# Kernel optimization log

Measured on AMD Instinct MI355X. Metric: run time of the kernel, lower is better.

Reference implementation:

```python
import jax, jax.numpy as jnp
import numpy as np

HEADS = 8
DIM_HEAD = 64
CHUNK = 128
EPS = 1e-6
KERNEL_EPS = 1e-4


def softmax_kernel(x, proj, is_query):
    # x: [b,h,n,d], proj: [f,d]  (FAVOR+ positive softmax features)
    d = x.shape[-1]
    data_normalizer = d ** -0.25
    ratio = proj.shape[0] ** -0.5
    data_dash = jnp.einsum('bhnd,fd->bhnf', x * data_normalizer, proj)
    diag = 0.5 * (data_normalizer ** 2) * jnp.sum(x * x, axis=-1, keepdims=True)  # [b,h,n,1]
    if is_query:
        m = jnp.max(data_dash, axis=-1, keepdims=True)
    else:
        m = jnp.max(data_dash, axis=(-1, -2), keepdims=True)
    return ratio * (jnp.exp(data_dash - diag - jax.lax.stop_gradient(m)) + KERNEL_EPS)


def infer_hidden_states(q, k, v, chunk_size=CHUNK):
    # q,k: [b,h,n,f], v: [b,h,n,e]; chunked causal linear attention with carried cumsums
    b, h, n, f = q.shape
    e = v.shape[-1]
    nc = n // chunk_size

    def to_chunks(t):
        return jnp.moveaxis(t.reshape(b, h, nc, chunk_size, t.shape[-1]), 2, 0)

    qs, ks, vs = to_chunks(q), to_chunks(k), to_chunks(v)

    def step(carry, inp):
        Z, S = carry  # [b,h,1,f], [b,h,1,f,e]
        qc, kc, vc = inp
        k_cum = Z + jnp.cumsum(kc, axis=2)                       # [b,h,c,f]
        D_inv = 1.0 / jnp.einsum('bhnf,bhnf->bhn', qc, k_cum + EPS)
        ctx = jnp.einsum('bhnf,bhne->bhnfe', kc, vc)             # [b,h,c,f,e]
        ctx_cum = S + jnp.cumsum(ctx, axis=2)
        out = jnp.einsum('bhnfe,bhnf,bhn->bhne', ctx_cum, qc, D_inv)
        return (k_cum[:, :, -1:], ctx_cum[:, :, -1:]), out

    init = (jnp.zeros((b, h, 1, f), q.dtype), jnp.zeros((b, h, 1, f, e), q.dtype))
    (Z, S), outs = jax.lax.scan(step, init, (qs, ks, vs))
    out = jnp.moveaxis(outs, 0, 2).reshape(b, h, n, e)
    return out, Z[:, :, 0], S[:, :, 0]


def reference(x, proj, Wq, Wk, Wv, Wo, bo):
    b, n, dim = x.shape
    h, dh = HEADS, DIM_HEAD

    def split_heads(t):
        return jnp.transpose(t.reshape(b, n, h, dh), (0, 2, 1, 3))

    q = split_heads(x @ Wq)
    k = split_heads(x @ Wk)
    v = split_heads(x @ Wv)

    qf = softmax_kernel(q, proj, is_query=True)
    kf = softmax_kernel(k, proj, is_query=False)

    out, Z, S = infer_hidden_states(qf, kf, v)
    out = jnp.transpose(out, (0, 2, 1, 3)).reshape(b, n, h * dh)
    out = out @ Wo + bo
    return out, Z, S


def setup_inputs() -> dict:
    key = jax.random.key(0)
    ks = jax.random.split(key, 6)
    b, n, dim = 2, 2048, 512
    f = 256
    return {
        'x': jax.random.normal(ks[0], (b, n, dim), jnp.float32),
        'proj': jax.random.normal(ks[1], (f, DIM_HEAD), jnp.float32),
        'Wq': jax.random.normal(ks[2], (dim, dim), jnp.float32) * (dim ** -0.5),
        'Wk': jax.random.normal(ks[3], (dim, dim), jnp.float32) * (dim ** -0.5),
        'Wv': jax.random.normal(ks[4], (dim, dim), jnp.float32) * (dim ** -0.5),
        'Wo': jax.random.normal(ks[5], (dim, dim), jnp.float32) * (dim ** -0.5),
        'bo': jnp.zeros((dim,), jnp.float32),
    }
```

## Files before the change

### kernel.cpp

```cpp
#include <hip/hip_runtime.h>
#include <hip/hip_bf16.h>
#include <math.h>

#define NB    2
#define NSEQ  2048
#define DIMM  512
#define NH    8
#define DHd   64
#define FF    256
#define CHK   128
#define NCHK  16
#define NBH   16

typedef unsigned short ushort_t;
typedef __attribute__((ext_vector_type(8))) __bf16 bf16x8;
typedef __attribute__((ext_vector_type(4))) float floatx4;

__device__ __forceinline__ unsigned short f2bf(float x) {
    union { __hip_bfloat16 h; unsigned short u; } v;
    v.h = __float2bfloat16(x);
    return v.u;
}
__device__ __forceinline__ float bf2f(unsigned short u) {
    union { unsigned short u2[2]; float f; } v;
    v.u2[0] = 0; v.u2[1] = u;
    return v.f;
}
__device__ __forceinline__ unsigned enc_f(float x) {
    unsigned u = __float_as_uint(x);
    return (u & 0x80000000u) ? ~u : (u | 0x80000000u);
}
__device__ __forceinline__ float dec_f(unsigned e) {
    unsigned u = (e & 0x80000000u) ? (e & 0x7fffffffu) : ~e;
    return __uint_as_float(u);
}

__device__ __forceinline__ void gload16(const void* g, void* l) {
    __builtin_amdgcn_global_load_lds(
        (const __attribute__((address_space(1))) void*)g,
        (__attribute__((address_space(3))) void*)l, 16, 0, 0);
}

__device__ __forceinline__ bf16x8 frag8(const ushort_t* lds, int row, int kb) {
    return *((const bf16x8*)lds + row * 8 + (kb ^ (row & 7)));
}
__device__ __forceinline__ bf16x8 fragS(const ushort_t* lds, int row, int kb) {
    return *((const bf16x8*)lds + row * 16 + (kb ^ (row & 15)));
}

__device__ __forceinline__ void stage8(const ushort_t* __restrict__ G, ushort_t* dst,
                                       int ld, int tid) {
#pragma unroll
    for (int t = 0; t < 4; t++) {
        const int g = t * 256 + tid, r = g >> 3, kb = (g & 7) ^ (r & 7);
        gload16(G + (size_t)r * ld + kb * 8, dst + (size_t)g * 8);
    }
}
__device__ __forceinline__ void stage4h(const ushort_t* __restrict__ G, ushort_t* dst,
                                        int ld, int tid) {
#pragma unroll
    for (int t = 0; t < 2; t++) {
        const int g = t * 256 + tid, r = g >> 3, kb = (g & 7) ^ (r & 7);
        gload16(G + (size_t)r * ld + kb * 8, dst + (size_t)g * 8);
    }
}
__device__ __forceinline__ void stageV(const ushort_t* __restrict__ G, ushort_t* dst,
                                       int tid) {
#pragma unroll
    for (int t = 0; t < 4; t++) {
        const int g = t * 256 + tid, r = g >> 4, kb = (g & 15) ^ (r & 15);
        gload16(G + (size_t)r * NSEQ + kb * 8, dst + (size_t)g * 8);
    }
}

__global__ __launch_bounds__(256)
void prep(const float* __restrict__ x, const float* __restrict__ proj,
          const float* __restrict__ W0, const float* __restrict__ W1,
          const float* __restrict__ W2, const float* __restrict__ W3,
          ushort_t* __restrict__ xb, ushort_t* __restrict__ projb,
          ushort_t* __restrict__ T0, ushort_t* __restrict__ T1,
          ushort_t* __restrict__ T2, ushort_t* __restrict__ T3,
          unsigned* __restrict__ mk_u)
{
    __shared__ float t[32][33];
    const int b = blockIdx.x, tid = threadIdx.x;
    if (b < 2048) {
        const int gid = b * 256 + tid;
        const float4 v = *(const float4*)(x + (size_t)gid * 4);
        union { ushort4 v4; unsigned short s[4]; } pk;
        pk.s[0] = f2bf(v.x); pk.s[1] = f2bf(v.y); pk.s[2] = f2bf(v.z); pk.s[3] = f2bf(v.w);
        ((ushort4*)xb)[gid] = pk.v4;
    } else if (b < 2064) {
        const int gid = (b - 2048) * 256 + tid;
        const float dn = 0.35355339059327379f;
        const float4 v = *(const float4*)(proj + (size_t)gid * 4);
        union { ushort4 v4; unsigned short s[4]; } pk;
        pk.s[0] = f2bf(v.x * dn); pk.s[1] = f2bf(v.y * dn);
        pk.s[2] = f2bf(v.z * dn); pk.s[3] = f2bf(v.w * dn);
        ((ushort4*)projb)[gid] = pk.v4;
    } else if (b < 3088) {
        const int idx = b - 2064;
        const int z = idx >> 8, rem = idx & 255;
        const int bx = rem & 15, by = rem >> 4;
        const float* W = (z == 0) ? W0 : (z == 1) ? W1 : (z == 2) ? W2 : W3;
        ushort_t* T = (z == 0) ? T0 : (z == 1) ? T1 : (z == 2) ? T2 : T3;
        const int x0 = bx * 32, y0 = by * 32;
        const int tx = tid & 31, ty = tid >> 5;
#pragma unroll
        for (int i = 0; i < 4; i++)
            t[ty + i * 8][tx] = W[(size_t)(y0 + ty + i * 8) * DIMM + x0 + tx];
        __syncthreads();
#pragma unroll
        for (int i = 0; i < 4; i++)
            T[(size_t)(x0 + ty + i * 8) * DIMM + y0 + tx] = f2bf(t[tx][ty + i * 8]);
    } else {
        if (tid < NBH) mk_u[tid] = 0u;
    }
}

__device__ __forceinline__ void mm44(const ushort_t* A, const ushort_t* B,
                                     floatx4 acc[4][4], int wm, int wn, int c, int q)
{
#pragma unroll
    for (int ks = 0; ks < 2; ks++) {
        bf16x8 af[4], bfr[4];
#pragma unroll
        for (int i = 0; i < 4; i++) {
            af[i]  = frag8(A, wm + i * 16 + c, ks * 4 + q);
            bfr[i] = frag8(B, wn + i * 16 + c, ks * 4 + q);
        }
#pragma unroll
        for (int i = 0; i < 4; i++)
#pragma unroll
            for (int j = 0; j < 4; j++)
                acc[i][j] = __builtin_amdgcn_mfma_f32_16x16x32_bf16(
                    af[i], bfr[j], acc[i][j], 0, 0, 0);
    }
}

__global__ __launch_bounds__(256)
void gemm_qkv(const ushort_t* __restrict__ xb,
              const ushort_t* __restrict__ Wtq, const ushort_t* __restrict__ Wtk,
              const ushort_t* __restrict__ Wtv, const ushort_t* __restrict__ projb,
              ushort_t* __restrict__ qb, ushort_t* __restrict__ kb,
              ushort_t* __restrict__ vTb, unsigned* __restrict__ mk_u)
{
    __shared__ alignas(16) ushort_t SM[33792];
    __shared__ float wred[2][4];
    ushort_t* A0 = SM;
    ushort_t* B0 = SM + 8192;
    ushort_t* A1 = SM + 16384;
    ushort_t* B1 = SM + 24576;
    ushort_t* PS = SM + 17408;
    const int tid = threadIdx.x;
    const int bid = blockIdx.x;
    const int z = bid % 3, tt = bid / 3;
    const int n0 = (tt & 3) * 128, m0 = (tt >> 2) * 128;
    const ushort_t* Bt = (z == 0) ? Wtq : ((z == 1) ? Wtk : Wtv);
    const ushort_t* AG = xb + (size_t)m0 * DIMM;
    const ushort_t* BG = Bt + (size_t)n0 * DIMM;

    const int lane = tid & 63, wid = tid >> 6;
    const int q = lane >> 4, cl = lane & 15;
    const int wm = (wid >> 1) * 64, wn = (wid & 1) * 64;

    floatx4 zero = {0.f, 0.f, 0.f, 0.f};
    floatx4 acc[4][4];
#pragma unroll
    for (int i = 0; i < 4; i++)
#pragma unroll
        for (int j = 0; j < 4; j++) acc[i][j] = zero;

    stage8(AG, A0, DIMM, tid);
    stage8(BG, B0, DIMM, tid);
    __syncthreads();
    for (int t4 = 0; t4 < 4; t4++) {
        const int k0 = t4 * 128;
        stage8(AG + k0 + 64, A1, DIMM, tid);
        stage8(BG + k0 + 64, B1, DIMM, tid);
        mm44(A0, B0, acc, wm, wn, cl, q);
        __syncthreads();
        if (t4 < 3) {
            stage8(AG + k0 + 128, A0, DIMM, tid);
            stage8(BG + k0 + 128, B0, DIMM, tid);
        }
        mm44(A1, B1, acc, wm, wn, cl, q);
        __syncthreads();
    }

    if (z == 1) {
        stage8(projb, PS, 64, tid);
        stage8(projb + 8192, PS + 8192, 64, tid);
    }

#pragma unroll
    for (int i = 0; i < 4; i++)
#pragma unroll
        for (int j = 0; j < 4; j++) {
            const int col = wn + j * 16 + cl;
#pragma unroll
            for (int r = 0; r < 4; r++) {
                const int row = wm + i * 16 + q * 4 + r;
                SM[row * 136 + col] = f2bf(acc[i][j][r]);
            }
        }
    __syncthreads();

    if (z < 2) {
        ushort_t* ob = (z == 0) ? qb : kb;
#pragma unroll
        for (int p = 0; p < 16; p++) {
            const int idx = p * 256 + tid;
            const int row = idx >> 5, c4 = idx & 31;
            ushort4 o = *(const ushort4*)&SM[row * 136 + c4 * 4];
            *(ushort4*)(ob + (size_t)(m0 + row) * DIMM + n0 + c4 * 4) = o;
        }
        if (z == 1) {
            const int bb = m0 >> 11;
            const int h0 = n0 >> 6;
            float mx[2] = {-3.0e38f, -3.0e38f};
#pragma unroll
            for (int hh = 0; hh < 2; hh++) {
#pragma unroll
                for (int half = 0; half < 2; half++) {
                    floatx4 a2[4][4];
#pragma unroll
                    for (int i = 0; i < 4; i++)
#pragma unroll
                        for (int j = 0; j < 4; j++) a2[i][j] = zero;
#pragma unroll
                    for (int ks = 0; ks < 2; ks++) {
                        bf16x8 af[4], bfr[4];
#pragma unroll
                        for (int i = 0; i < 4; i++)
                            af[i] = *(const bf16x8*)&SM[(wm + i * 16 + cl) * 136 + hh * 64 + (ks * 4 + q) * 8];
#pragma unroll
                        for (int j = 0; j < 4; j++)
                            bfr[j] = frag8(PS + half * 8192, wn + j * 16 + cl, ks * 4 + q);
#pragma unroll
                        for (int i = 0; i < 4; i++)
#pragma unroll
                            for (int j = 0; j < 4; j++)
                                a2[i][j] = __builtin_amdgcn_mfma_f32_16x16x32_bf16(
                                    af[i], bfr[j], a2[i][j], 0, 0, 0);
                    }
#pragma unroll
                    for (int i = 0; i < 4; i++)
#pragma unroll
                        for (int j = 0; j < 4; j++)
#pragma unroll
                            for (int r = 0; r < 4; r++) mx[hh] = fmaxf(mx[hh], a2[i][j][r]);
                }
            }
#pragma unroll
            for (int hh = 0; hh < 2; hh++) {
                float m = mx[hh];
                m = fmaxf(m, __shfl_xor(m, 1));  m = fmaxf(m, __shfl_xor(m, 2));
                m = fmaxf(m, __shfl_xor(m, 4));  m = fmaxf(m, __shfl_xor(m, 8));
                m = fmaxf(m, __shfl_xor(m, 16)); m = fmaxf(m, __shfl_xor(m, 32));
                if (lane == 0) wred[hh][wid] = m;
            }
            __syncthreads();
            if (tid == 0) {
#pragma unroll
                for (int hh = 0; hh < 2; hh++) {
                    const float m = fmaxf(fmaxf(wred[hh][0], wred[hh][1]),
                                          fmaxf(wred[hh][2], wred[hh][3]));
                    atomicMax(&mk_u[bb * NH + h0 + hh], enc_f(m));
                }
            }
        }
    } else {
        const int bb = m0 >> 11, nbase = m0 & 2047;
#pragma unroll
        for (int p = 0; p < 16; p++) {
            const int idx = p * 256 + tid;
            const int cl2 = idx >> 5, n4 = idx & 31;
            const int C = n0 + cl2;
            const int h = C >> 6, e = C & 63;
            union { ushort4 v4; unsigned short s[4]; } pk;
#pragma unroll
            for (int k = 0; k < 4; k++) pk.s[k] = SM[(n4 * 4 + k) * 136 + cl2];
            *(ushort4*)(vTb + (((size_t)(bb * NH + h) * 64 + e)) * NSEQ + nbase + n4 * 4) = pk.v4;
        }
    }
}

__device__ __forceinline__ void mm24(const ushort_t* A, const ushort_t* B,
                                     floatx4 acc[2][4], int wm, int wn, int c, int q)
{
#pragma unroll
    for (int ks = 0; ks < 2; ks++) {
        bf16x8 af[2], bfr[4];
#pragma unroll
        for (int i = 0; i < 2; i++) af[i] = frag8(A, wm + i * 16 + c, ks * 4 + q);
#pragma unroll
        for (int j = 0; j < 4; j++) bfr[j] = frag8(B, wn + j * 16 + c, ks * 4 + q);
#pragma unroll
        for (int i = 0; i < 2; i++)
#pragma unroll
            for (int j = 0; j < 4; j++)
                acc[i][j] = __builtin_amdgcn_mfma_f32_16x16x32_bf16(
                    af[i], bfr[j], acc[i][j], 0, 0, 0);
    }
}

__global__ __launch_bounds__(256)
void gemm_out(const ushort_t* __restrict__ attnb, const ushort_t* __restrict__ Wto,
              float* __restrict__ out, const float* __restrict__ bias)
{
    __shared__ alignas(16) ushort_t A0[4096];
    __shared__ alignas(16) ushort_t A1[4096];
    __shared__ alignas(16) ushort_t B0[8192];
    __shared__ alignas(16) ushort_t B1[8192];
    const int tid = threadIdx.x;
    const int n0 = blockIdx.x * 128, m0 = blockIdx.y * 64;
    const ushort_t* AG = attnb + (size_t)m0 * DIMM;
    const ushort_t* BG = Wto + (size_t)n0 * DIMM;

    floatx4 zero = {0.f, 0.f, 0.f, 0.f};
    floatx4 acc[2][4];
#pragma unroll
    for (int i = 0; i < 2; i++)
#pragma unroll
        for (int j = 0; j < 4; j++) acc[i][j] = zero;

    const int lane = tid & 63, wid = tid >> 6;
    const int q = lane >> 4, c = lane & 15;
    const int wm = (wid >> 1) * 32, wn = (wid & 1) * 64;

    stage4h(AG, A0, DIMM, tid);
    stage8(BG, B0, DIMM, tid);
    __syncthreads();
    for (int tt = 0; tt < 4; tt++) {
        const int k0 = tt * 128;
        stage4h(AG + k0 + 64, A1, DIMM, tid);
        stage8(BG + k0 + 64, B1, DIMM, tid);
        mm24(A0, B0, acc, wm, wn, c, q);
        __syncthreads();
        if (tt < 3) {
            stage4h(AG + k0 + 128, A0, DIMM, tid);
            stage8(BG + k0 + 128, B0, DIMM, tid);
        }
        mm24(A1, B1, acc, wm, wn, c, q);
        __syncthreads();
    }

#pragma unroll
    for (int i = 0; i < 2; i++)
#pragma unroll
        for (int j = 0; j < 4; j++) {
            const int col = n0 + wn + j * 16 + c;
            const float bv = bias[col];
#pragma unroll
            for (int r = 0; r < 4; r++) {
                const int row = m0 + wm + i * 16 + q * 4 + r;
                out[(size_t)row * DIMM + col] = acc[i][j][r] + bv;
            }
        }
}

__global__ __launch_bounds__(256)
void featk(const ushort_t* __restrict__ kb_, const ushort_t* __restrict__ projb,
           const unsigned* __restrict__ mk_u, const ushort_t* __restrict__ vTb,
           ushort_t* __restrict__ kfb, float* __restrict__ CTXT,
           float* __restrict__ Ksum)
{
    __shared__ alignas(16) ushort_t SM[17408];
    __shared__ alignas(16) ushort_t Vs[8192];
    __shared__ float dtmp[256];
    __shared__ float diag_l[128];
    __shared__ float colp[2][128];
    ushort_t* As = SM;
    ushort_t* Bs = SM + 8192;
    const int tid = threadIdx.x, lane = tid & 63, wid = tid >> 6;
    const int q = lane >> 4, cl = lane & 15;
    const int m0 = blockIdx.x * 128, h = blockIdx.y, fh = blockIdx.z;
    const int bb = m0 >> 11, nloc = m0 & 2047;
    const int bh = bb * NH + h;
    const int cidx = nloc >> 7;
    const ushort_t* Aq = kb_ + (size_t)m0 * DIMM + h * 64;
    const ushort_t* Vg = vTb + ((size_t)bh * 64) * NSEQ + nloc;
    const ushort_t* Pj = projb + (size_t)fh * 128 * 64;

    {
        const int row = tid >> 1, half = tid & 1;
        float s = 0.f;
        const ushort_t* p = Aq + (size_t)row * DIMM + half * 32;
#pragma unroll
        for (int d = 0; d < 32; d += 4) {
            ushort4 w = *(const ushort4*)(p + d);
            float a = bf2f(w.x), b2 = bf2f(w.y), c2 = bf2f(w.z), d2 = bf2f(w.w);
            s += a * a + b2 * b2 + c2 * c2 + d2 * d2;
        }
        dtmp[tid] = s;
    }
    stage8(Aq, As, DIMM, tid);
    stage8(Pj, Bs, 64, tid);
    stageV(Vg, Vs, tid);
    __syncthreads();
    if (tid < 128) diag_l[tid] = (dtmp[2 * tid] + dtmp[2 * tid + 1]) * 0.0625f;

    floatx4 zero = {0.f, 0.f, 0.f, 0.f};
    floatx4 acc[4][4];
#pragma unroll
    for (int i = 0; i < 4; i++)
#pragma unroll
        for (int j = 0; j < 4; j++) acc[i][j] = zero;
    const int wm = (wid >> 1) * 64, wn = (wid & 1) * 64;
#pragma unroll
    for (int ks = 0; ks < 2; ks++) {
        bf16x8 af[4], bfr[4];
#pragma unroll
        for (int i = 0; i < 4; i++) af[i] = frag8(As, wm + i * 16 + cl, ks * 4 + q);
#pragma unroll
        for (int j = 0; j < 4; j++) bfr[j] = frag8(Bs, wn + j * 16 + cl, ks * 4 + q);
#pragma unroll
        for (int i = 0; i < 4; i++)
#pragma unroll
            for (int j = 0; j < 4; j++)
                acc[i][j] = __builtin_amdgcn_mfma_f32_16x16x32_bf16(
                    af[i], bfr[j], acc[i][j], 0, 0, 0);
    }
    __syncthreads();

    const float mk = dec_f(mk_u[bh]);
#pragma unroll
    for (int i = 0; i < 4; i++)
#pragma unroll
        for (int r = 0; r < 4; r++) {
            const int row = wm + i * 16 + q * 4 + r;
            const float cc = diag_l[row] + mk;
#pragma unroll
            for (int j = 0; j < 4; j++)
                acc[i][j][r] = 0.0625f * (__expf(acc[i][j][r] - cc) + 1.0e-4f);
        }

#pragma unroll
    for (int j = 0; j < 4; j++) {
        float s = 0.f;
#pragma unroll
        for (int i = 0; i < 4; i++)
            s += acc[i][j][0] + acc[i][j][1] + acc[i][j][2] + acc[i][j][3];
        s += __shfl_xor(s, 16);
        s += __shfl_xor(s, 32);
        if (q == 0) colp[wid >> 1][wn + j * 16 + cl] = s;
    }

#pragma unroll
    for (int i = 0; i < 4; i++)
#pragma unroll
        for (int j = 0; j < 4; j++) {
            const int col = wn + j * 16 + cl;
#pragma unroll
            for (int r = 0; r < 4; r++) {
                const int row = wm + i * 16 + q * 4 + r;
                SM[row * 136 + col] = f2bf(acc[i][j][r]);
            }
        }
    __syncthreads();

    if (tid < 128)
        Ksum[((size_t)bh * NCHK + cidx) * FF + fh * 128 + tid] = colp[0][tid] + colp[1][tid];

    const size_t frow = (size_t)bh * NSEQ + nloc;
#pragma unroll
    for (int p = 0; p < 16; p++) {
        const int idx = p * 256 + tid;
        const int row = idx >> 5, c4 = idx & 31;
        ushort4 o = *(const ushort4*)&SM[row * 136 + c4 * 4];
        *(ushort4*)(kfb + (frow + row) * FF + fh * 128 + c4 * 4) = o;
    }
    __syncthreads();

    ushort_t* T = SM;
    const size_t cbase = ((size_t)bh * NCHK + cidx) * 64;
#pragma unroll
    for (int fq = 0; fq < 2; fq++) {
        if ((wid & 1) == fq) {
#pragma unroll
            for (int jj = 0; jj < 4; jj++) {
#pragma unroll
                for (int i = 0; i < 4; i++)
#pragma unroll
                    for (int r = 0; r < 4; r++) {
                        const int n = wm + i * 16 + q * 4 + r;
                        T[(jj * 16 + cl) * 136 + n] = f2bf(acc[i][jj][r]);
                    }
            }
        }
        __syncthreads();
        floatx4 accc[4];
#pragma unroll
        for (int jj = 0; jj < 4; jj++) accc[jj] = zero;
#pragma unroll
        for (int kt = 0; kt < 4; kt++) {
            const bf16x8 av = fragS(Vs, wid * 16 + cl, kt * 4 + q);
#pragma unroll
            for (int jj = 0; jj < 4; jj++) {
                const bf16x8 bv = *(const bf16x8*)(T + (jj * 16 + cl) * 136 + (kt * 4 + q) * 8);
                accc[jj] = __builtin_amdgcn_mfma_f32_16x16x32_bf16(av, bv, accc[jj], 0, 0, 0);
            }
        }
#pragma unroll
        for (int jj = 0; jj < 4; jj++) {
            const int f = fh * 128 + fq * 64 + jj * 16 + cl;
#pragma unroll
            for (int r = 0; r < 4; r++) {
                const int e = wid * 16 + q * 4 + r;
                CTXT[(cbase + e) * FF + f] = accc[jj][r];
            }
        }
        __syncthreads();
    }
}

__global__ void prefix_zs(float* __restrict__ Ksum, float* __restrict__ Zout,
                          const float* __restrict__ CTXT, ushort_t* __restrict__ ctxp,
                          float* __restrict__ Sout)
{
    const int b = blockIdx.x;
    if (b < 1024) {
        const int idx = b * 256 + threadIdx.x;
        const int bh = idx >> 14, ef = idx & 16383;
        const int e = ef >> 8, f = ef & 255;
        float run = 0.f;
#pragma unroll
        for (int c = 0; c < NCHK; c++) {
            const size_t o = (((size_t)bh * NCHK + c) * 64 + e) * FF + f;
            const float t = CTXT[o];
            ctxp[o] = f2bf(run);
            run += t;
        }
        Sout[((size_t)bh * FF + f) * 64 + e] = run;
    } else {
        const int idx = (b - 1024) * 256 + threadIdx.x;
        const int bh = idx >> 8, f = idx & 255;
        float run = 0.f;
#pragma unroll
        for (int c = 0; c < NCHK; c++) {
            const size_t o = ((size_t)(bh * NCHK + c)) * FF + f;
            const float t = Ksum[o];
            Ksum[o] = run;
            run += t;
        }
        Zout[(size_t)bh * FF + f] = run;
    }
}

template<int NJ>
__device__ __forceinline__ void st1N(const ushort_t* QFs, const ushort_t* Bk,
                                     floatx4* acc1, int wv, int cl, int q)
{
#pragma unroll
    for (int ks = 0; ks < 2; ks++) {
        const bf16x8 af = frag8(QFs, wv * 16 + cl, ks * 4 + q);
        bf16x8 bfr[NJ];
#pragma unroll
        for (int j = 0; j < NJ; j++) bfr[j] = frag8(Bk, j * 16 + cl, ks * 4 + q);
#pragma unroll
        for (int j = 0; j < NJ; j++)
            acc1[j] = __builtin_amdgcn_mfma_f32_16x16x32_bf16(af, bfr[j], acc1[j], 0, 0, 0);
    }
}

__device__ __forceinline__ void pv4(const ushort_t* CpB, const ushort_t* QFs,
                                    floatx4 acc2[4], int wv, int cl, int q)
{
#pragma unroll
    for (int ks = 0; ks < 2; ks++) {
        const bf16x8 bfr = frag8(QFs, wv * 16 + cl, ks * 4 + q);
#pragma unroll
        for (int i = 0; i < 4; i++) {
            const bf16x8 af = frag8(CpB, i * 16 + cl, ks * 4 + q);
            acc2[i] = __builtin_amdgcn_mfma_f32_16x16x32_bf16(af, bfr, acc2[i], 0, 0, 0);
        }
    }
}

__global__ __launch_bounds__(256)
void chunk_out_half(const ushort_t* __restrict__ qb_, const ushort_t* __restrict__ projb,
                    const ushort_t* __restrict__ kfb, const ushort_t* __restrict__ vTb,
                    const float* __restrict__ Zex, const ushort_t* __restrict__ ctxp,
                    ushort_t* __restrict__ attnb)
{
    __shared__ alignas(16) ushort_t QF[16384];
    __shared__ alignas(16) ushort_t BufA[8192];
    __shared__ alignas(16) ushort_t Ssl[8192];
    __shared__ alignas(16) ushort_t BufB[4096];
    __shared__ float zeps[256];
    __shared__ float dtmp[256];
    __shared__ float diag_l[64];
    __shared__ float rows_part[64];
    __shared__ float denp[256];
    __shared__ float den_l[64];

    const int tid = threadIdx.x, lane = tid & 63, wv = tid >> 6;
    const int q = lane >> 4, cl = lane & 15;
    const int bh = blockIdx.x >> 5, r5 = blockIdx.x & 31;
    const int c = r5 >> 1, hq = r5 & 1;
    const int bb = bh >> 3, h = bh & 7;
    const int n0 = c * CHK, q0 = n0 + hq * 64;
    const ushort_t* Kf = kfb + ((size_t)bh * NSEQ + n0) * FF;
    const ushort_t* Aq = qb_ + ((size_t)(bb * NSEQ + q0)) * DIMM + h * 64;
    const ushort_t* Vt = vTb + ((size_t)bh * 64) * NSEQ + n0;
    const ushort_t* Cp = ctxp + ((size_t)bh * NCHK + c) * 64 * FF;

    zeps[tid] = Zex[((size_t)bh * NCHK + c) * FF + tid] + 1.0e-6f;

    stage4h(Aq, BufB, DIMM, tid);
    stage8(projb, BufA, 64, tid);
    stage8(projb + 128 * 64, Ssl, 64, tid);
    {
        const int row = tid >> 2, qd = tid & 3;
        float s = 0.f;
        const ushort_t* p = Aq + (size_t)row * DIMM + qd * 16;
#pragma unroll
        for (int d = 0; d < 16; d += 4) {
            ushort4 w = *(const ushort4*)(p + d);
            float a = bf2f(w.x), b2 = bf2f(w.y), c2 = bf2f(w.z), d2 = bf2f(w.w);
            s += a * a + b2 * b2 + c2 * c2 + d2 * d2;
        }
        dtmp[tid] = s;
    }
    __syncthreads();
    if (tid < 64)
        diag_l[tid] = (dtmp[4 * tid] + dtmp[4 * tid + 1] +
                       dtmp[4 * tid + 2] + dtmp[4 * tid + 3]) * 0.0625f;

    floatx4 zero = {0.f, 0.f, 0.f, 0.f};
    floatx4 accqA[8], accqB[8];
#pragma unroll
    for (int j = 0; j < 8; j++) { accqA[j] = zero; accqB[j] = zero; }
#pragma unroll
    for (int ks = 0; ks < 2; ks++) {
        const bf16x8 af = frag8(BufB, wv * 16 + cl, ks * 4 + q);
#pragma unroll
        for (int j = 0; j < 8; j++) {
            const bf16x8 b0 = frag8(BufA, j * 16 + cl, ks * 4 + q);
            accqA[j] = __builtin_amdgcn_mfma_f32_16x16x32_bf16(af, b0, accqA[j], 0, 0, 0);
        }
#pragma unroll
        for (int j = 0; j < 8; j++) {
            const bf16x8 b1 = frag8(Ssl, j * 16 + cl, ks * 4 + q);
            accqB[j] = __builtin_amdgcn_mfma_f32_16x16x32_bf16(af, b1, accqB[j], 0, 0, 0);
        }
    }
    float rmax[4];
#pragma unroll
    for (int r = 0; r < 4; r++) {
        float m = -3.0e38f;
#pragma unroll
        for (int j = 0; j < 8; j++) m = fmaxf(m, fmaxf(accqA[j][r], accqB[j][r]));
        m = fmaxf(m, __shfl_xor(m, 1)); m = fmaxf(m, __shfl_xor(m, 2));
        m = fmaxf(m, __shfl_xor(m, 4)); m = fmaxf(m, __shfl_xor(m, 8));
        rmax[r] = m;
    }
    __syncthreads();
#pragma unroll
    for (int r = 0; r < 4; r++) {
        const int rowL = wv * 16 + q * 4 + r;
        const float cc = diag_l[rowL] + rmax[r];
#pragma unroll
        for (int j = 0; j < 8; j++) {
            {
                const int col = j * 16 + cl;
                const float v = 0.0625f * (__expf(accqA[j][r] - cc) + 1.0e-4f);
                const int s = col >> 6, fp = col & 63;
                QF[s * 4096 + (rowL * 8 + ((fp >> 3) ^ (rowL & 7))) * 8 + (fp & 7)] = f2bf(v);
            }
            {
                const int col = 128 + j * 16 + cl;
                const float v = 0.0625f * (__expf(accqB[j][r] - cc) + 1.0e-4f);
                const int s = col >> 6, fp = col & 63;
                QF[s * 4096 + (rowL * 8 + ((fp >> 3) ^ (rowL & 7))) * 8 + (fp & 7)] = f2bf(v);
            }
        }
    }
    if (hq) stage8(Kf, Ssl, FF, tid); else stage4h(Kf, Ssl, FF, tid);
    __syncthreads();

    floatx4 acc1[8];
#pragma unroll
    for (int j = 0; j < 8; j++) acc1[j] = zero;
    if (hq) {
        stage8(Kf + 64, BufA, FF, tid);
        st1N<8>(QF, Ssl, acc1, wv, cl, q);
        __syncthreads();
        stage8(Kf + 128, Ssl, FF, tid);
        st1N<8>(QF + 4096, BufA, acc1, wv, cl, q);
        __syncthreads();
        stage8(Kf + 192, BufA, FF, tid);
        st1N<8>(QF + 8192, Ssl, acc1, wv, cl, q);
        __syncthreads();
        st1N<8>(QF + 12288, BufA, acc1, wv, cl, q);
    } else {
        stage4h(Kf + 64, BufA, FF, tid);
        st1N<4>(QF, Ssl, acc1, wv, cl, q);
        __syncthreads();
        stage4h(Kf + 128, Ssl, FF, tid);
        st1N<4>(QF + 4096, BufA, acc1, wv, cl, q);
        __syncthreads();
        stage4h(Kf + 192, BufA, FF, tid);
        st1N<4>(QF + 8192, Ssl, acc1, wv, cl, q);
        __syncthreads();
        st1N<4>(QF + 12288, BufA, acc1, wv, cl, q);
    }

    if (hq) {
#pragma unroll
        for (int r = 0; r < 4; r++) {
            const int rowL = wv * 16 + q * 4 + r;
            const int rowG = 64 + rowL;
            float part = 0.f;
#pragma unroll
            for (int j = 0; j < 8; j++) {
                const int col = j * 16 + cl;
                const float v = (col <= rowG) ? acc1[j][r] : 0.f;
                part += v;
                Ssl[(rowL * 16 + ((col >> 3) ^ (rowL & 15))) * 8 + (col & 7)] = f2bf(v);
            }
            part += __shfl_xor(part, 1); part += __shfl_xor(part, 2);
            part += __shfl_xor(part, 4); part += __shfl_xor(part, 8);
            if (cl == 0) rows_part[rowL] = part;
        }
    } else {
#pragma unroll
        for (int r = 0; r < 4; r++) {
            const int rowL = wv * 16 + q * 4 + r;
            float part = 0.f;
#pragma unroll
            for (int j = 0; j < 4; j++) {
                const int col = j * 16 + cl;
                const float v = (col <= rowL) ? acc1[j][r] : 0.f;
                part += v;
                Ssl[(rowL * 16 + ((col >> 3) ^ (rowL & 15))) * 8 + (col & 7)] = f2bf(v);
            }
            part += __shfl_xor(part, 1); part += __shfl_xor(part, 2);
            part += __shfl_xor(part, 4); part += __shfl_xor(part, 8);
            if (cl == 0) rows_part[rowL] = part;
        }
    }
    __syncthreads();

    if (hq) stageV(Vt, BufA, tid); else stage4h(Vt, BufA, NSEQ, tid);
    stage4h(Cp, BufB, FF, tid);
    float dacc = 0.f;
    {
        const int drow = tid >> 2, dq = tid & 3;
        const ushort_t* QQ = QF + dq * 4096;
#pragma unroll
        for (int gi = 0; gi < 8; gi++) {
            const ushort_t* gp = QQ + ((size_t)drow * 8 + (gi ^ (drow & 7))) * 8;
            const int kbase = dq * 64 + gi * 8;
#pragma unroll
            for (int e2 = 0; e2 < 8; e2++)
                dacc = fmaf(bf2f(gp[e2]), zeps[kbase + e2], dacc);
        }
    }
    __syncthreads();

    floatx4 acc2[4];
#pragma unroll
    for (int i = 0; i < 4; i++) acc2[i] = zero;
    if (hq) {
#pragma unroll
        for (int kk = 0; kk < 4; kk++) {
            const bf16x8 bfr = fragS(Ssl, wv * 16 + cl, kk * 4 + q);
#pragma unroll
            for (int i = 0; i < 4; i++) {
                const bf16x8 af = fragS(BufA, i * 16 + cl, kk * 4 + q);
                acc2[i] = __builtin_amdgcn_mfma_f32_16x16x32_bf16(af, bfr, acc2[i], 0, 0, 0);
            }
        }
    } else {
#pragma unroll
        for (int kk = 0; kk < 2; kk++) {
            const bf16x8 bfr = fragS(Ssl, wv * 16 + cl, kk * 4 + q);
#pragma unroll
            for (int i = 0; i < 4; i++) {
                const bf16x8 af = frag8(BufA, i * 16 + cl, kk * 4 + q);
                acc2[i] = __builtin_amdgcn_mfma_f32_16x16x32_bf16(af, bfr, acc2[i], 0, 0, 0);
            }
        }
    }
    denp[tid] = dacc;
    __syncthreads();

    stage4h(Cp + 64, BufA, FF, tid);
    stage4h(Cp + 128, BufA + 4096, FF, tid);
    pv4(BufB, QF, acc2, wv, cl, q);
    __syncthreads();
    stage4h(Cp + 192, BufB, FF, tid);
    pv4(BufA, QF + 4096, acc2, wv, cl, q);
    pv4(BufA + 4096, QF + 8192, acc2, wv, cl, q);
    if (tid < 64)
        den_l[tid] = rows_part[tid] + denp[4 * tid] + denp[4 * tid + 1] +
                     denp[4 * tid + 2] + denp[4 * tid + 3];
    __syncthreads();
    pv4(BufB, QF + 12288, acc2, wv, cl, q);

    const float dinv = 1.0f / den_l[wv * 16 + cl];
#pragma unroll
    for (int i = 0; i < 4; i++)
#pragma unroll
        for (int r = 0; r < 4; r++) {
            const int e = i * 16 + q * 4 + r;
            Ssl[(wv * 16 + cl) * 68 + e] = f2bf(acc2[i][r] * dinv);
        }
    __syncthreads();
#pragma unroll
    for (int p = 0; p < 4; p++) {
        const int idx = p * 256 + tid;
        const int row = idx >> 4, e4 = idx & 15;
        ushort4 o = *(const ushort4*)&Ssl[row * 68 + e4 * 4];
        *(ushort4*)(attnb + ((size_t)(bb * NSEQ + q0 + row)) * DIMM + h * 64 + e4 * 4) = o;
    }
}

extern "C" void kernel_launch(void* const* d_in, const int* in_sizes, int n_in,
                              void* d_out, int out_size, void* d_ws, size_t ws_size,
                              hipStream_t stream)
{
    (void)in_sizes; (void)n_in; (void)out_size; (void)ws_size;
    const float* x    = (const float*)d_in[0];
    const float* proj = (const float*)d_in[1];
    const float* Wq   = (const float*)d_in[2];
    const float* Wk   = (const float*)d_in[3];
    const float* Wv   = (const float*)d_in[4];
    const float* Wo   = (const float*)d_in[5];
    const float* bo   = (const float*)d_in[6];
    float* out = (float*)d_out;

    char* W = (char*)d_ws;
    float*    CTXT = (float*)W;              W += (size_t)16777216;
    ushort_t* kfb  = (ushort_t*)W;           W += (size_t)16777216;
    ushort_t* ctxp = (ushort_t*)W;           W += (size_t)8388608;
    ushort_t* qb   = (ushort_t*)W;           W += (size_t)4194304;
    ushort_t* kb   = (ushort_t*)W;           W += (size_t)4194304;
    ushort_t* xb   = (ushort_t*)W;           W += (size_t)4194304;
    ushort_t* vTb  = (ushort_t*)W;           W += (size_t)4194304;
    ushort_t* Wtq  = (ushort_t*)W;           W += (size_t)524288;
    ushort_t* Wtk  = (ushort_t*)W;           W += (size_t)524288;
    ushort_t* Wtv  = (ushort_t*)W;           W += (size_t)524288;
    ushort_t* Wto  = (ushort_t*)W;           W += (size_t)524288;
    ushort_t* projb = (ushort_t*)W;          W += (size_t)32768;
    float*    Ksum = (float*)W;              W += (size_t)262144;
    unsigned* mk_u = (unsigned*)W;           W += (size_t)256;

    ushort_t* attnb = xb;

    float* Zout = out + (size_t)4096 * 512;
    float* Sout = Zout + (size_t)NBH * FF;

    hipLaunchKernelGGL(prep, dim3(3089), dim3(256), 0, stream,
                       x, proj, Wq, Wk, Wv, Wo, xb, projb, Wtq, Wtk, Wtv, Wto, mk_u);
    hipLaunchKernelGGL(gemm_qkv, dim3(384), dim3(256), 0, stream,
                       xb, Wtq, Wtk, Wtv, projb, qb, kb, vTb, mk_u);
    hipLaunchKernelGGL(featk, dim3(32, 8, 2), dim3(256), 0, stream,
                       kb, projb, mk_u, vTb, kfb, CTXT, Ksum);
    hipLaunchKernelGGL(prefix_zs, dim3(1040), dim3(256), 0, stream,
                       Ksum, Zout, CTXT, ctxp, Sout);
    hipLaunchKernelGGL(chunk_out_half, dim3(512), dim3(256), 0, stream,
                       qb, projb, kfb, vTb, Ksum, ctxp, attnb);
    hipLaunchKernelGGL(gemm_out, dim3(4, 64), dim3(256), 0, stream, attnb, Wto, out, bo);
}
```

Measured before the change: 135.3 us.

## Fuse attention tail kernels into one persistent kernel with grid barriers

Replaces the four launches featk, prefix_zs, chunk_out_half and gemm_out with a single 512-block persistent kernel whose phases are separated by software grid barriers built on atomic counters and flags. This removes three kernel launches and the idle gaps between them. The output GEMM is retiled to 64x64 so it maps onto 512 blocks. The cost is spin-wait barriers that need all 512 blocks resident at once (launch bounds 256,2). That co-residency is not guaranteed and could deadlock, and the smaller GEMM tiles may be less efficient.

```diff
diff --git a/kernel.cpp b/kernel.cpp
--- a/kernel.cpp
+++ b/kernel.cpp
@@ -71,6 +71,25 @@
         const int g = t * 256 + tid, r = g >> 4, kb = (g & 15) ^ (r & 15);
         gload16(G + (size_t)r * NSEQ + kb * 8, dst + (size_t)g * 8);
     }
+}
+
+__device__ __forceinline__ void gbar(unsigned* bar, int idx, unsigned nblk, int tid)
+{
+    __threadfence();
+    __syncthreads();
+    if (tid == 0) {
+        unsigned* cnt = bar + idx * 2;
+        unsigned* flg = bar + idx * 2 + 1;
+        unsigned v = __hip_atomic_fetch_add(cnt, 1u, __ATOMIC_ACQ_REL, __HIP_MEMORY_SCOPE_AGENT);
+        if (v + 1u == nblk) {
+            __hip_atomic_store(flg, 1u, __ATOMIC_RELEASE, __HIP_MEMORY_SCOPE_AGENT);
+        } else {
+            while (__hip_atomic_load(flg, __ATOMIC_ACQUIRE, __HIP_MEMORY_SCOPE_AGENT) == 0u)
+                __builtin_amdgcn_s_sleep(16);
+        }
+    }
+    __syncthreads();
+    __threadfence();
 }
 
 __global__ __launch_bounds__(256)
@@ -114,7 +133,7 @@
         for (int i = 0; i < 4; i++)
             T[(size_t)(x0 + ty + i * 8) * DIMM + y0 + tx] = f2bf(t[tx][ty + i * 8]);
     } else {
-        if (tid < NBH) mk_u[tid] = 0u;
+        if (tid < 24) mk_u[tid] = 0u;
     }
 }
 
@@ -133,6 +152,25 @@
         for (int i = 0; i < 4; i++)
 #pragma unroll
             for (int j = 0; j < 4; j++)
+                acc[i][j] = __builtin_amdgcn_mfma_f32_16x16x32_bf16(
+                    af[i], bfr[j], acc[i][j], 0, 0, 0);
+    }
+}
+__device__ __forceinline__ void mm22(const ushort_t* A, const ushort_t* B,
+                                     floatx4 acc[2][2], int wm, int wn, int c, int q)
+{
+#pragma unroll
+    for (int ks = 0; ks < 2; ks++) {
+        bf16x8 af[2], bfr[2];
+#pragma unroll
+        for (int i = 0; i < 2; i++) {
+            af[i]  = frag8(A, wm + i * 16 + c, ks * 4 + q);
+            bfr[i] = frag8(B, wn + i * 16 + c, ks * 4 + q);
+        }
+#pragma unroll
+        for (int i = 0; i < 2; i++)
+#pragma unroll
+            for (int j = 0; j < 2; j++)
                 acc[i][j] = __builtin_amdgcn_mfma_f32_16x16x32_bf16(
                     af[i], bfr[j], acc[i][j], 0, 0, 0);
     }
@@ -286,268 +324,6 @@
     }
 }
 
-__device__ __forceinline__ void mm24(const ushort_t* A, const ushort_t* B,
-                                     floatx4 acc[2][4], int wm, int wn, int c, int q)
-{
-#pragma unroll
-    for (int ks = 0; ks < 2; ks++) {
-        bf16x8 af[2], bfr[4];
-#pragma unroll
-        for (int i = 0; i < 2; i++) af[i] = frag8(A, wm + i * 16 + c, ks * 4 + q);
-#pragma unroll
-        for (int j = 0; j < 4; j++) bfr[j] = frag8(B, wn + j * 16 + c, ks * 4 + q);
-#pragma unroll
-        for (int i = 0; i < 2; i++)
-#pragma unroll
-            for (int j = 0; j < 4; j++)
-                acc[i][j] = __builtin_amdgcn_mfma_f32_16x16x32_bf16(
-                    af[i], bfr[j], acc[i][j], 0, 0, 0);
-    }
-}
-
-__global__ __launch_bounds__(256)
-void gemm_out(const ushort_t* __restrict__ attnb, const ushort_t* __restrict__ Wto,
-              float* __restrict__ out, const float* __restrict__ bias)
-{
-    __shared__ alignas(16) ushort_t A0[4096];
-    __shared__ alignas(16) ushort_t A1[4096];
-    __shared__ alignas(16) ushort_t B0[8192];
-    __shared__ alignas(16) ushort_t B1[8192];
-    const int tid = threadIdx.x;
-    const int n0 = blockIdx.x * 128, m0 = blockIdx.y * 64;
-    const ushort_t* AG = attnb + (size_t)m0 * DIMM;
-    const ushort_t* BG = Wto + (size_t)n0 * DIMM;
-
-    floatx4 zero = {0.f, 0.f, 0.f, 0.f};
-    floatx4 acc[2][4];
-#pragma unroll
-    for (int i = 0; i < 2; i++)
-#pragma unroll
-        for (int j = 0; j < 4; j++) acc[i][j] = zero;
-
-    const int lane = tid & 63, wid = tid >> 6;
-    const int q = lane >> 4, c = lane & 15;
-    const int wm = (wid >> 1) * 32, wn = (wid & 1) * 64;
-
-    stage4h(AG, A0, DIMM, tid);
-    stage8(BG, B0, DIMM, tid);
-    __syncthreads();
-    for (int tt = 0; tt < 4; tt++) {
-        const int k0 = tt * 128;
-        stage4h(AG + k0 + 64, A1, DIMM, tid);
-        stage8(BG + k0 + 64, B1, DIMM, tid);
-        mm24(A0, B0, acc, wm, wn, c, q);
-        __syncthreads();
-        if (tt < 3) {
-            stage4h(AG + k0 + 128, A0, DIMM, tid);
-            stage8(BG + k0 + 128, B0, DIMM, tid);
-        }
-        mm24(A1, B1, acc, wm, wn, c, q);
-        __syncthreads();
-    }
-
-#pragma unroll
-    for (int i = 0; i < 2; i++)
-#pragma unroll
-        for (int j = 0; j < 4; j++) {
-            const int col = n0 + wn + j * 16 + c;
-            const float bv = bias[col];
-#pragma unroll
-            for (int r = 0; r < 4; r++) {
-                const int row = m0 + wm + i * 16 + q * 4 + r;
-                out[(size_t)row * DIMM + col] = acc[i][j][r] + bv;
-            }
-        }
-}
-
-__global__ __launch_bounds__(256)
-void featk(const ushort_t* __restrict__ kb_, const ushort_t* __restrict__ projb,
-           const unsigned* __restrict__ mk_u, const ushort_t* __restrict__ vTb,
-           ushort_t* __restrict__ kfb, float* __restrict__ CTXT,
-           float* __restrict__ Ksum)
-{
-    __shared__ alignas(16) ushort_t SM[17408];
-    __shared__ alignas(16) ushort_t Vs[8192];
-    __shared__ float dtmp[256];
-    __shared__ float diag_l[128];
-    __shared__ float colp[2][128];
-    ushort_t* As = SM;
-    ushort_t* Bs = SM + 8192;
-    const int tid = threadIdx.x, lane = tid & 63, wid = tid >> 6;
-    const int q = lane >> 4, cl = lane & 15;
-    const int m0 = blockIdx.x * 128, h = blockIdx.y, fh = blockIdx.z;
-    const int bb = m0 >> 11, nloc = m0 & 2047;
-    const int bh = bb * NH + h;
-    const int cidx = nloc >> 7;
-    const ushort_t* Aq = kb_ + (size_t)m0 * DIMM + h * 64;
-    const ushort_t* Vg = vTb + ((size_t)bh * 64) * NSEQ + nloc;
-    const ushort_t* Pj = projb + (size_t)fh * 128 * 64;
-
-    {
-        const int row = tid >> 1, half = tid & 1;
-        float s = 0.f;
-        const ushort_t* p = Aq + (size_t)row * DIMM + half * 32;
-#pragma unroll
-        for (int d = 0; d < 32; d += 4) {
-            ushort4 w = *(const ushort4*)(p + d);
-            float a = bf2f(w.x), b2 = bf2f(w.y), c2 = bf2f(w.z), d2 = bf2f(w.w);
-            s += a * a + b2 * b2 + c2 * c2 + d2 * d2;
-        }
-        dtmp[tid] = s;
-    }
-    stage8(Aq, As, DIMM, tid);
-    stage8(Pj, Bs, 64, tid);
-    stageV(Vg, Vs, tid);
-    __syncthreads();
-    if (tid < 128) diag_l[tid] = (dtmp[2 * tid] + dtmp[2 * tid + 1]) * 0.0625f;
-
-    floatx4 zero = {0.f, 0.f, 0.f, 0.f};
-    floatx4 acc[4][4];
-#pragma unroll
-    for (int i = 0; i < 4; i++)
-#pragma unroll
-        for (int j = 0; j < 4; j++) acc[i][j] = zero;
-    const int wm = (wid >> 1) * 64, wn = (wid & 1) * 64;
-#pragma unroll
-    for (int ks = 0; ks < 2; ks++) {
-        bf16x8 af[4], bfr[4];
-#pragma unroll
-        for (int i = 0; i < 4; i++) af[i] = frag8(As, wm + i * 16 + cl, ks * 4 + q);
-#pragma unroll
-        for (int j = 0; j < 4; j++) bfr[j] = frag8(Bs, wn + j * 16 + cl, ks * 4 + q);
-#pragma unroll
-        for (int i = 0; i < 4; i++)
-#pragma unroll
-            for (int j = 0; j < 4; j++)
-                acc[i][j] = __builtin_amdgcn_mfma_f32_16x16x32_bf16(
-                    af[i], bfr[j], acc[i][j], 0, 0, 0);
-    }
-    __syncthreads();
-
-    const float mk = dec_f(mk_u[bh]);
-#pragma unroll
-    for (int i = 0; i < 4; i++)
-#pragma unroll
-        for (int r = 0; r < 4; r++) {
-            const int row = wm + i * 16 + q * 4 + r;
-            const float cc = diag_l[row] + mk;
-#pragma unroll
-            for (int j = 0; j < 4; j++)
-                acc[i][j][r] = 0.0625f * (__expf(acc[i][j][r] - cc) + 1.0e-4f);
-        }
-
-#pragma unroll
-    for (int j = 0; j < 4; j++) {
-        float s = 0.f;
-#pragma unroll
-        for (int i = 0; i < 4; i++)
-            s += acc[i][j][0] + acc[i][j][1] + acc[i][j][2] + acc[i][j][3];
-        s += __shfl_xor(s, 16);
-        s += __shfl_xor(s, 32);
-        if (q == 0) colp[wid >> 1][wn + j * 16 + cl] = s;
-    }
-
-#pragma unroll
-    for (int i = 0; i < 4; i++)
-#pragma unroll
-        for (int j = 0; j < 4; j++) {
-            const int col = wn + j * 16 + cl;
-#pragma unroll
-            for (int r = 0; r < 4; r++) {
-                const int row = wm + i * 16 + q * 4 + r;
-                SM[row * 136 + col] = f2bf(acc[i][j][r]);
-            }
-        }
-    __syncthreads();
-
-    if (tid < 128)
-        Ksum[((size_t)bh * NCHK + cidx) * FF + fh * 128 + tid] = colp[0][tid] + colp[1][tid];
-
-    const size_t frow = (size_t)bh * NSEQ + nloc;
-#pragma unroll
-    for (int p = 0; p < 16; p++) {
-        const int idx = p * 256 + tid;
-        const int row = idx >> 5, c4 = idx & 31;
-        ushort4 o = *(const ushort4*)&SM[row * 136 + c4 * 4];
-        *(ushort4*)(kfb + (frow + row) * FF + fh * 128 + c4 * 4) = o;
-    }
-    __syncthreads();
-
-    ushort_t* T = SM;
-    const size_t cbase = ((size_t)bh * NCHK + cidx) * 64;
-#pragma unroll
-    for (int fq = 0; fq < 2; fq++) {
-        if ((wid & 1) == fq) {
-#pragma unroll
-            for (int jj = 0; jj < 4; jj++) {
-#pragma unroll
-                for (int i = 0; i < 4; i++)
-#pragma unroll
-                    for (int r = 0; r < 4; r++) {
-                        const int n = wm + i * 16 + q * 4 + r;
-                        T[(jj * 16 + cl) * 136 + n] = f2bf(acc[i][jj][r]);
-                    }
-            }
-        }
-        __syncthreads();
-        floatx4 accc[4];
-#pragma unroll
-        for (int jj = 0; jj < 4; jj++) accc[jj] = zero;
-#pragma unroll
-        for (int kt = 0; kt < 4; kt++) {
-            const bf16x8 av = fragS(Vs, wid * 16 + cl, kt * 4 + q);
-#pragma unroll
-            for (int jj = 0; jj < 4; jj++) {
-                const bf16x8 bv = *(const bf16x8*)(T + (jj * 16 + cl) * 136 + (kt * 4 + q) * 8);
-                accc[jj] = __builtin_amdgcn_mfma_f32_16x16x32_bf16(av, bv, accc[jj], 0, 0, 0);
-            }
-        }
-#pragma unroll
-        for (int jj = 0; jj < 4; jj++) {
-            const int f = fh * 128 + fq * 64 + jj * 16 + cl;
-#pragma unroll
-            for (int r = 0; r < 4; r++) {
-                const int e = wid * 16 + q * 4 + r;
-                CTXT[(cbase + e) * FF + f] = accc[jj][r];
-            }
-        }
-        __syncthreads();
-    }
-}
-
-__global__ void prefix_zs(float* __restrict__ Ksum, float* __restrict__ Zout,
-                          const float* __restrict__ CTXT, ushort_t* __restrict__ ctxp,
-                          float* __restrict__ Sout)
-{
-    const int b = blockIdx.x;
-    if (b < 1024) {
-        const int idx = b * 256 + threadIdx.x;
-        const int bh = idx >> 14, ef = idx & 16383;
-        const int e = ef >> 8, f = ef & 255;
-        float run = 0.f;
-#pragma unroll
-        for (int c = 0; c < NCHK; c++) {
-            const size_t o = (((size_t)bh * NCHK + c) * 64 + e) * FF + f;
-            const float t = CTXT[o];
-            ctxp[o] = f2bf(run);
-            run += t;
-        }
-        Sout[((size_t)bh * FF + f) * 64 + e] = run;
-    } else {
-        const int idx = (b - 1024) * 256 + threadIdx.x;
-        const int bh = idx >> 8, f = idx & 255;
-        float run = 0.f;
-#pragma unroll
-        for (int c = 0; c < NCHK; c++) {
-            const size_t o = ((size_t)(bh * NCHK + c)) * FF + f;
-            const float t = Ksum[o];
-            Ksum[o] = run;
-            run += t;
-        }
-        Zout[(size_t)bh * FF + f] = run;
-    }
-}
-
 template<int NJ>
 __device__ __forceinline__ void st1N(const ushort_t* QFs, const ushort_t* Bk,
                                      floatx4* acc1, int wv, int cl, int q)
@@ -578,243 +354,481 @@
     }
 }
 
-__global__ __launch_bounds__(256)
-void chunk_out_half(const ushort_t* __restrict__ qb_, const ushort_t* __restrict__ projb,
-                    const ushort_t* __restrict__ kfb, const ushort_t* __restrict__ vTb,
-                    const float* __restrict__ Zex, const ushort_t* __restrict__ ctxp,
-                    ushort_t* __restrict__ attnb)
+#define NBLK 512u
+
+__global__ __launch_bounds__(256, 2)
+void tail_fused(const ushort_t* __restrict__ kb_, const ushort_t* __restrict__ projb,
+                const unsigned* __restrict__ mk_u, const ushort_t* __restrict__ vTb,
+                ushort_t* __restrict__ kfb, float* __restrict__ CTXT,
+                float* __restrict__ Ksum, float* __restrict__ Zout,
+                ushort_t* __restrict__ ctxp, float* __restrict__ Sout,
+                const ushort_t* __restrict__ qb_, ushort_t* __restrict__ attnb,
+                const ushort_t* __restrict__ Wto, float* __restrict__ out,
+                const float* __restrict__ bias, unsigned* __restrict__ bar)
 {
-    __shared__ alignas(16) ushort_t QF[16384];
-    __shared__ alignas(16) ushort_t BufA[8192];
-    __shared__ alignas(16) ushort_t Ssl[8192];
-    __shared__ alignas(16) ushort_t BufB[4096];
-    __shared__ float zeps[256];
-    __shared__ float dtmp[256];
-    __shared__ float diag_l[64];
-    __shared__ float rows_part[64];
-    __shared__ float denp[256];
-    __shared__ float den_l[64];
-
-    const int tid = threadIdx.x, lane = tid & 63, wv = tid >> 6;
+    __shared__ alignas(16) char SMEM[77824];
+    const int tid = threadIdx.x, bid = blockIdx.x;
+    const int lane = tid & 63, wid = tid >> 6;
     const int q = lane >> 4, cl = lane & 15;
-    const int bh = blockIdx.x >> 5, r5 = blockIdx.x & 31;
-    const int c = r5 >> 1, hq = r5 & 1;
-    const int bb = bh >> 3, h = bh & 7;
-    const int n0 = c * CHK, q0 = n0 + hq * 64;
-    const ushort_t* Kf = kfb + ((size_t)bh * NSEQ + n0) * FF;
-    const ushort_t* Aq = qb_ + ((size_t)(bb * NSEQ + q0)) * DIMM + h * 64;
-    const ushort_t* Vt = vTb + ((size_t)bh * 64) * NSEQ + n0;
-    const ushort_t* Cp = ctxp + ((size_t)bh * NCHK + c) * 64 * FF;
-
-    zeps[tid] = Zex[((size_t)bh * NCHK + c) * FF + tid] + 1.0e-6f;
-
-    stage4h(Aq, BufB, DIMM, tid);
-    stage8(projb, BufA, 64, tid);
-    stage8(projb + 128 * 64, Ssl, 64, tid);
+    floatx4 zero = {0.f, 0.f, 0.f, 0.f};
+
     {
-        const int row = tid >> 2, qd = tid & 3;
-        float s = 0.f;
-        const ushort_t* p = Aq + (size_t)row * DIMM + qd * 16;
-#pragma unroll
-        for (int d = 0; d < 16; d += 4) {
-            ushort4 w = *(const ushort4*)(p + d);
-            float a = bf2f(w.x), b2 = bf2f(w.y), c2 = bf2f(w.z), d2 = bf2f(w.w);
-            s += a * a + b2 * b2 + c2 * c2 + d2 * d2;
-        }
-        dtmp[tid] = s;
-    }
-    __syncthreads();
-    if (tid < 64)
-        diag_l[tid] = (dtmp[4 * tid] + dtmp[4 * tid + 1] +
-                       dtmp[4 * tid + 2] + dtmp[4 * tid + 3]) * 0.0625f;
-
-    floatx4 zero = {0.f, 0.f, 0.f, 0.f};
-    floatx4 accqA[8], accqB[8];
-#pragma unroll
-    for (int j = 0; j < 8; j++) { accqA[j] = zero; accqB[j] = zero; }
-#pragma unroll
-    for (int ks = 0; ks < 2; ks++) {
-        const bf16x8 af = frag8(BufB, wv * 16 + cl, ks * 4 + q);
-#pragma unroll
-        for (int j = 0; j < 8; j++) {
-            const bf16x8 b0 = frag8(BufA, j * 16 + cl, ks * 4 + q);
-            accqA[j] = __builtin_amdgcn_mfma_f32_16x16x32_bf16(af, b0, accqA[j], 0, 0, 0);
-        }
-#pragma unroll
-        for (int j = 0; j < 8; j++) {
-            const bf16x8 b1 = frag8(Ssl, j * 16 + cl, ks * 4 + q);
-            accqB[j] = __builtin_amdgcn_mfma_f32_16x16x32_bf16(af, b1, accqB[j], 0, 0, 0);
-        }
-    }
-    float rmax[4];
-#pragma unroll
-    for (int r = 0; r < 4; r++) {
-        float m = -3.0e38f;
-#pragma unroll
-        for (int j = 0; j < 8; j++) m = fmaxf(m, fmaxf(accqA[j][r], accqB[j][r]));
-        m = fmaxf(m, __shfl_xor(m, 1)); m = fmaxf(m, __shfl_xor(m, 2));
-        m = fmaxf(m, __shfl_xor(m, 4)); m = fmaxf(m, __shfl_xor(m, 8));
-        rmax[r] = m;
-    }
-    __syncthreads();
-#pragma unroll
-    for (int r = 0; r < 4; r++) {
-        const int rowL = wv * 16 + q * 4 + r;
-        const float cc = diag_l[rowL] + rmax[r];
-#pragma unroll
-        for (int j = 0; j < 8; j++) {
-            {
-                const int col = j * 16 + cl;
-                const float v = 0.0625f * (__expf(accqA[j][r] - cc) + 1.0e-4f);
-                const int s = col >> 6, fp = col & 63;
-                QF[s * 4096 + (rowL * 8 + ((fp >> 3) ^ (rowL & 7))) * 8 + (fp & 7)] = f2bf(v);
-            }
-            {
-                const int col = 128 + j * 16 + cl;
-                const float v = 0.0625f * (__expf(accqB[j][r] - cc) + 1.0e-4f);
-                const int s = col >> 6, fp = col & 63;
-                QF[s * 4096 + (rowL * 8 + ((fp >> 3) ^ (rowL & 7))) * 8 + (fp & 7)] = f2bf(v);
-            }
-        }
-    }
-    if (hq) stage8(Kf, Ssl, FF, tid); else stage4h(Kf, Ssl, FF, tid);
-    __syncthreads();
-
-    floatx4 acc1[8];
-#pragma unroll
-    for (int j = 0; j < 8; j++) acc1[j] = zero;
-    if (hq) {
-        stage8(Kf + 64, BufA, FF, tid);
-        st1N<8>(QF, Ssl, acc1, wv, cl, q);
-        __syncthreads();
-        stage8(Kf + 128, Ssl, FF, tid);
-        st1N<8>(QF + 4096, BufA, acc1, wv, cl, q);
-        __syncthreads();
-        stage8(Kf + 192, BufA, FF, tid);
-        st1N<8>(QF + 8192, Ssl, acc1, wv, cl, q);
-        __syncthreads();
-        st1N<8>(QF + 12288, BufA, acc1, wv, cl, q);
-    } else {
-        stage4h(Kf + 64, BufA, FF, tid);
-        st1N<4>(QF, Ssl, acc1, wv, cl, q);
-        __syncthreads();
-        stage4h(Kf + 128, Ssl, FF, tid);
-        st1N<4>(QF + 4096, BufA, acc1, wv, cl, q);
-        __syncthreads();
-        stage4h(Kf + 192, BufA, FF, tid);
-        st1N<4>(QF + 8192, Ssl, acc1, wv, cl, q);
-        __syncthreads();
-        st1N<4>(QF + 12288, BufA, acc1, wv, cl, q);
-    }
-
-    if (hq) {
+        ushort_t* SM = (ushort_t*)SMEM;
+        ushort_t* Vs = (ushort_t*)(SMEM + 34816);
+        float* dtmp   = (float*)(SMEM + 51200);
+        float* diag_l = (float*)(SMEM + 52224);
+        float (*colp)[128] = (float(*)[128])(SMEM + 52736);
+        ushort_t* As = SM;
+        ushort_t* Bs = SM + 8192;
+        const int cx = bid & 31, h = (bid >> 5) & 7, fh = bid >> 8;
+        const int m0 = cx * 128;
+        const int bb = m0 >> 11, nloc = m0 & 2047;
+        const int bh = bb * NH + h;
+        const int cidx = nloc >> 7;
+        const ushort_t* Aq = kb_ + (size_t)m0 * DIMM + h * 64;
+        const ushort_t* Vg = vTb + ((size_t)bh * 64) * NSEQ + nloc;
+        const ushort_t* Pj = projb + (size_t)fh * 128 * 64;
+
+        {
+            const int row = tid >> 1, half = tid & 1;
+            float s = 0.f;
+            const ushort_t* p = Aq + (size_t)row * DIMM + half * 32;
+#pragma unroll
+            for (int d = 0; d < 32; d += 4) {
+                ushort4 w = *(const ushort4*)(p + d);
+                float a = bf2f(w.x), b2 = bf2f(w.y), c2 = bf2f(w.z), d2 = bf2f(w.w);
+                s += a * a + b2 * b2 + c2 * c2 + d2 * d2;
+            }
+            dtmp[tid] = s;
+        }
+        stage8(Aq, As, DIMM, tid);
+        stage8(Pj, Bs, 64, tid);
+        stageV(Vg, Vs, tid);
+        __syncthreads();
+        if (tid < 128) diag_l[tid] = (dtmp[2 * tid] + dtmp[2 * tid + 1]) * 0.0625f;
+
+        floatx4 acc[4][4];
+#pragma unroll
+        for (int i = 0; i < 4; i++)
+#pragma unroll
+            for (int j = 0; j < 4; j++) acc[i][j] = zero;
+        const int wm = (wid >> 1) * 64, wn = (wid & 1) * 64;
+#pragma unroll
+        for (int ks = 0; ks < 2; ks++) {
+            bf16x8 af[4], bfr[4];
+#pragma unroll
+            for (int i = 0; i < 4; i++) af[i] = frag8(As, wm + i * 16 + cl, ks * 4 + q);
+#pragma unroll
+            for (int j = 0; j < 4; j++) bfr[j] = frag8(Bs, wn + j * 16 + cl, ks * 4 + q);
+#pragma unroll
+            for (int i = 0; i < 4; i++)
+#pragma unroll
+                for (int j = 0; j < 4; j++)
+                    acc[i][j] = __builtin_amdgcn_mfma_f32_16x16x32_bf16(
+                        af[i], bfr[j], acc[i][j], 0, 0, 0);
+        }
+        __syncthreads();
+
+        const float mk = dec_f(mk_u[bh]);
+#pragma unroll
+        for (int i = 0; i < 4; i++)
+#pragma unroll
+            for (int r = 0; r < 4; r++) {
+                const int row = wm + i * 16 + q * 4 + r;
+                const float cc = diag_l[row] + mk;
+#pragma unroll
+                for (int j = 0; j < 4; j++)
+                    acc[i][j][r] = 0.0625f * (__expf(acc[i][j][r] - cc) + 1.0e-4f);
+            }
+
+#pragma unroll
+        for (int j = 0; j < 4; j++) {
+            float s = 0.f;
+#pragma unroll
+            for (int i = 0; i < 4; i++)
+                s += acc[i][j][0] + acc[i][j][1] + acc[i][j][2] + acc[i][j][3];
+            s += __shfl_xor(s, 16);
+            s += __shfl_xor(s, 32);
+            if (q == 0) colp[wid >> 1][wn + j * 16 + cl] = s;
+        }
+
+#pragma unroll
+        for (int i = 0; i < 4; i++)
+#pragma unroll
+            for (int j = 0; j < 4; j++) {
+                const int col = wn + j * 16 + cl;
+#pragma unroll
+                for (int r = 0; r < 4; r++) {
+                    const int row = wm + i * 16 + q * 4 + r;
+                    SM[row * 136 + col] = f2bf(acc[i][j][r]);
+                }
+            }
+        __syncthreads();
+
+        if (tid < 128)
+            Ksum[((size_t)bh * NCHK + cidx) * FF + fh * 128 + tid] = colp[0][tid] + colp[1][tid];
+
+        const size_t frow = (size_t)bh * NSEQ + nloc;
+#pragma unroll
+        for (int p = 0; p < 16; p++) {
+            const int idx = p * 256 + tid;
+            const int row = idx >> 5, c4 = idx & 31;
+            ushort4 o = *(const ushort4*)&SM[row * 136 + c4 * 4];
+            *(ushort4*)(kfb + (frow + row) * FF + fh * 128 + c4 * 4) = o;
+        }
+        __syncthreads();
+
+        ushort_t* T = SM;
+        const size_t cbase = ((size_t)bh * NCHK + cidx) * 64;
+#pragma unroll
+        for (int fq = 0; fq < 2; fq++) {
+            if ((wid & 1) == fq) {
+#pragma unroll
+                for (int jj = 0; jj < 4; jj++) {
+#pragma unroll
+                    for (int i = 0; i < 4; i++)
+#pragma unroll
+                        for (int r = 0; r < 4; r++) {
+                            const int n = wm + i * 16 + q * 4 + r;
+                            T[(jj * 16 + cl) * 136 + n] = f2bf(acc[i][jj][r]);
+                        }
+                }
+            }
+            __syncthreads();
+            floatx4 accc[4];
+#pragma unroll
+            for (int jj = 0; jj < 4; jj++) accc[jj] = zero;
+#pragma unroll
+            for (int kt = 0; kt < 4; kt++) {
+                const bf16x8 av = fragS(Vs, wid * 16 + cl, kt * 4 + q);
+#pragma unroll
+                for (int jj = 0; jj < 4; jj++) {
+                    const bf16x8 bv = *(const bf16x8*)(T + (jj * 16 + cl) * 136 + (kt * 4 + q) * 8);
+                    accc[jj] = __builtin_amdgcn_mfma_f32_16x16x32_bf16(av, bv, accc[jj], 0, 0, 0);
+                }
+            }
+#pragma unroll
+            for (int jj = 0; jj < 4; jj++) {
+                const int f = fh * 128 + fq * 64 + jj * 16 + cl;
+#pragma unroll
+                for (int r = 0; r < 4; r++) {
+                    const int e = wid * 16 + q * 4 + r;
+                    CTXT[(cbase + e) * FF + f] = accc[jj][r];
+                }
+            }
+            __syncthreads();
+        }
+    }
+    gbar(bar, 0, NBLK, tid);
+
+    for (int w = bid; w < 1040; w += 512) {
+        if (w < 1024) {
+            const int idx = w * 256 + tid;
+            const int bh = idx >> 14, ef = idx & 16383;
+            const int e = ef >> 8, f = ef & 255;
+            float run = 0.f;
+#pragma unroll
+            for (int c = 0; c < NCHK; c++) {
+                const size_t o = (((size_t)bh * NCHK + c) * 64 + e) * FF + f;
+                const float t = CTXT[o];
+                ctxp[o] = f2bf(run);
+                run += t;
+            }
+            Sout[((size_t)bh * FF + f) * 64 + e] = run;
+        } else {
+            const int idx = (w - 1024) * 256 + tid;
+            const int bh = idx >> 8, f = idx & 255;
+            float run = 0.f;
+#pragma unroll
+            for (int c = 0; c < NCHK; c++) {
+                const size_t o = ((size_t)(bh * NCHK + c)) * FF + f;
+                const float t = Ksum[o];
+                Ksum[o] = run;
+                run += t;
+            }
+            Zout[(size_t)bh * FF + f] = run;
+        }
+    }
+    gbar(bar, 1, NBLK, tid);
+
+    {
+        ushort_t* QF   = (ushort_t*)SMEM;
+        ushort_t* BufA = (ushort_t*)(SMEM + 32768);
+        ushort_t* Ssl  = (ushort_t*)(SMEM + 49152);
+        ushort_t* BufB = (ushort_t*)(SMEM + 65536);
+        float* zeps      = (float*)(SMEM + 73728);
+        float* dtmp      = (float*)(SMEM + 74752);
+        float* diag_l    = (float*)(SMEM + 75776);
+        float* rows_part = (float*)(SMEM + 76032);
+        float* denp      = (float*)(SMEM + 76288);
+        float* den_l     = (float*)(SMEM + 77312);
+        const int wv = wid;
+        const int bh = bid >> 5, r5 = bid & 31;
+        const int c = r5 >> 1, hq = r5 & 1;
+        const int bb = bh >> 3, h = bh & 7;
+        const int n0 = c * CHK, q0 = n0 + hq * 64;
+        const ushort_t* Kf = kfb + ((size_t)bh * NSEQ + n0) * FF;
+        const ushort_t* Aq = qb_ + ((size_t)(bb * NSEQ + q0)) * DIMM + h * 64;
+        const ushort_t* Vt = vTb + ((size_t)bh * 64) * NSEQ + n0;
+        const ushort_t* Cp = ctxp + ((size_t)bh * NCHK + c) * 64 * FF;
+
+        zeps[tid] = Ksum[((size_t)bh * NCHK + c) * FF + tid] + 1.0e-6f;
+
+        stage4h(Aq, BufB, DIMM, tid);
+        stage8(projb, BufA, 64, tid);
+        stage8(projb + 128 * 64, Ssl, 64, tid);
+        {
+            const int row = tid >> 2, qd = tid & 3;
+            float s = 0.f;
+            const ushort_t* p = Aq + (size_t)row * DIMM + qd * 16;
+#pragma unroll
+            for (int d = 0; d < 16; d += 4) {
+                ushort4 w = *(const ushort4*)(p + d);
+                float a = bf2f(w.x), b2 = bf2f(w.y), c2 = bf2f(w.z), d2 = bf2f(w.w);
+                s += a * a + b2 * b2 + c2 * c2 + d2 * d2;
+            }
+            dtmp[tid] = s;
+        }
+        __syncthreads();
+        if (tid < 64)
+            diag_l[tid] = (dtmp[4 * tid] + dtmp[4 * tid + 1] +
+                           dtmp[4 * tid + 2] + dtmp[4 * tid + 3]) * 0.0625f;
+
+        floatx4 accqA[8], accqB[8];
+#pragma unroll
+        for (int j = 0; j < 8; j++) { accqA[j] = zero; accqB[j] = zero; }
+#pragma unroll
+        for (int ks = 0; ks < 2; ks++) {
+            const bf16x8 af = frag8(BufB, wv * 16 + cl, ks * 4 + q);
+#pragma unroll
+            for (int j = 0; j < 8; j++) {
+                const bf16x8 b0 = frag8(BufA, j * 16 + cl, ks * 4 + q);
+                accqA[j] = __builtin_amdgcn_mfma_f32_16x16x32_bf16(af, b0, accqA[j], 0, 0, 0);
+            }
+#pragma unroll
+            for (int j = 0; j < 8; j++) {
+                const bf16x8 b1 = frag8(Ssl, j * 16 + cl, ks * 4 + q);
+                accqB[j] = __builtin_amdgcn_mfma_f32_16x16x32_bf16(af, b1, accqB[j], 0, 0, 0);
+            }
+        }
+        float rmax[4];
+#pragma unroll
+        for (int r = 0; r < 4; r++) {
+            float m = -3.0e38f;
+#pragma unroll
+            for (int j = 0; j < 8; j++) m = fmaxf(m, fmaxf(accqA[j][r], accqB[j][r]));
+            m = fmaxf(m, __shfl_xor(m, 1)); m = fmaxf(m, __shfl_xor(m, 2));
+            m = fmaxf(m, __shfl_xor(m, 4)); m = fmaxf(m, __shfl_xor(m, 8));
+            rmax[r] = m;
+        }
+        __syncthreads();
 #pragma unroll
         for (int r = 0; r < 4; r++) {
             const int rowL = wv * 16 + q * 4 + r;
-            const int rowG = 64 + rowL;
-            float part = 0.f;
+            const float cc = diag_l[rowL] + rmax[r];
 #pragma unroll
             for (int j = 0; j < 8; j++) {
-                const int col = j * 16 + cl;
-                const float v = (col <= rowG) ? acc1[j][r] : 0.f;
-                part += v;
-                Ssl[(rowL * 16 + ((col >> 3) ^ (rowL & 15))) * 8 + (col & 7)] = f2bf(v);
-            }
-            part += __shfl_xor(part, 1); part += __shfl_xor(part, 2);
-            part += __shfl_xor(part, 4); part += __shfl_xor(part, 8);
-            if (cl == 0) rows_part[rowL] = part;
-        }
-    } else {
-#pragma unroll
-        for (int r = 0; r < 4; r++) {
-            const int rowL = wv * 16 + q * 4 + r;
-            float part = 0.f;
-#pragma unroll
-            for (int j = 0; j < 4; j++) {
-                const int col = j * 16 + cl;
-                const float v = (col <= rowL) ? acc1[j][r] : 0.f;
-                part += v;
-                Ssl[(rowL * 16 + ((col >> 3) ^ (rowL & 15))) * 8 + (col & 7)] = f2bf(v);
-            }
-            part += __shfl_xor(part, 1); part += __shfl_xor(part, 2);
-            part += __shfl_xor(part, 4); part += __shfl_xor(part, 8);
-            if (cl == 0) rows_part[rowL] = part;
-        }
-    }
-    __syncthreads();
-
-    if (hq) stageV(Vt, BufA, tid); else stage4h(Vt, BufA, NSEQ, tid);
-    stage4h(Cp, BufB, FF, tid);
-    float dacc = 0.f;
+                {
+                    const int col = j * 16 + cl;
+                    const float v = 0.0625f * (__expf(accqA[j][r] - cc) + 1.0e-4f);
+                    const int s = col >> 6, fp = col & 63;
+                    QF[s * 4096 + (rowL * 8 + ((fp >> 3) ^ (rowL & 7))) * 8 + (fp & 7)] = f2bf(v);
+                }
+                {
+                    const int col = 128 + j * 16 + cl;
+                    const float v = 0.0625f * (__expf(accqB[j][r] - cc) + 1.0e-4f);
+                    const int s = col >> 6, fp = col & 63;
+                    QF[s * 4096 + (rowL * 8 + ((fp >> 3) ^ (rowL & 7))) * 8 + (fp & 7)] = f2bf(v);
+                }
+            }
+        }
+        if (hq) stage8(Kf, Ssl, FF, tid); else stage4h(Kf, Ssl, FF, tid);
+        __syncthreads();
+
+        floatx4 acc1[8];
+#pragma unroll
+        for (int j = 0; j < 8; j++) acc1[j] = zero;
+        if (hq) {
+            stage8(Kf + 64, BufA, FF, tid);
+            st1N<8>(QF, Ssl, acc1, wv, cl, q);
+            __syncthreads();
+            stage8(Kf + 128, Ssl, FF, tid);
+            st1N<8>(QF + 4096, BufA, acc1, wv, cl, q);
+            __syncthreads();
+            stage8(Kf + 192, BufA, FF, tid);
+            st1N<8>(QF + 8192, Ssl, acc1, wv, cl, q);
+            __syncthreads();
+            st1N<8>(QF + 12288, BufA, acc1, wv, cl, q);
+        } else {
+            stage4h(Kf + 64, BufA, FF, tid);
+            st1N<4>(QF, Ssl, acc1, wv, cl, q);
+            __syncthreads();
+            stage4h(Kf + 128, Ssl, FF, tid);
+            st1N<4>(QF + 4096, BufA, acc1, wv, cl, q);
+            __syncthreads();
+            stage4h(Kf + 192, BufA, FF, tid);
+            st1N<4>(QF + 8192, Ssl, acc1, wv, cl, q);
+            __syncthreads();
+            st1N<4>(QF + 12288, BufA, acc1, wv, cl, q);
+        }
+
+        if (hq) {
+#pragma unroll
+            for (int r = 0; r < 4; r++) {
+                const int rowL = wv * 16 + q * 4 + r;
+                const int rowG = 64 + rowL;
+                float part = 0.f;
+#pragma unroll
+                for (int j = 0; j < 8; j++) {
+                    const int col = j * 16 + cl;
+                    const float v = (col <= rowG) ? acc1[j][r] : 0.f;
+                    part += v;
+                    Ssl[(rowL * 16 + ((col >> 3) ^ (rowL & 15))) * 8 + (col & 7)] = f2bf(v);
+                }
+                part += __shfl_xor(part, 1); part += __shfl_xor(part, 2);
+                part += __shfl_xor(part, 4); part += __shfl_xor(part, 8);
+                if (cl == 0) rows_part[rowL] = part;
+            }
+        } else {
+#pragma unroll
+            for (int r = 0; r < 4; r++) {
+                const int rowL = wv * 16 + q * 4 + r;
+                float part = 0.f;
+#pragma unroll
+                for (int j = 0; j < 4; j++) {
+                    const int col = j * 16 + cl;
+                    const float v = (col <= rowL) ? acc1[j][r] : 0.f;
+                    part += v;
+                    Ssl[(rowL * 16 + ((col >> 3) ^ (rowL & 15))) * 8 + (col & 7)] = f2bf(v);
+                }
+                part += __shfl_xor(part, 1); part += __shfl_xor(part, 2);
+                part += __shfl_xor(part, 4); part += __shfl_xor(part, 8);
+                if (cl == 0) rows_part[rowL] = part;
+            }
+        }
+        __syncthreads();
+
+        if (hq) stageV(Vt, BufA, tid); else stage4h(Vt, BufA, NSEQ, tid);
+        stage4h(Cp, BufB, FF, tid);
+        float dacc = 0.f;
+        {
+            const int drow = tid >> 2, dq = tid & 3;
+            const ushort_t* QQ = QF + dq * 4096;
+#pragma unroll
+            for (int gi = 0; gi < 8; gi++) {
+                const ushort_t* gp = QQ + ((size_t)drow * 8 + (gi ^ (drow & 7))) * 8;
+                const int kbase = dq * 64 + gi * 8;
+#pragma unroll
+                for (int e2 = 0; e2 < 8; e2++)
+                    dacc = fmaf(bf2f(gp[e2]), zeps[kbase + e2], dacc);
+            }
+        }
+        __syncthreads();
+
+        floatx4 acc2[4];
+#pragma unroll
+        for (int i = 0; i < 4; i++) acc2[i] = zero;
+        if (hq) {
+#pragma unroll
+            for (int kk = 0; kk < 4; kk++) {
+                const bf16x8 bfr = fragS(Ssl, wv * 16 + cl, kk * 4 + q);
+#pragma unroll
+                for (int i = 0; i < 4; i++) {
+                    const bf16x8 af = fragS(BufA, i * 16 + cl, kk * 4 + q);
+                    acc2[i] = __builtin_amdgcn_mfma_f32_16x16x32_bf16(af, bfr, acc2[i], 0, 0, 0);
+                }
+            }
+        } else {
+#pragma unroll
+            for (int kk = 0; kk < 2; kk++) {
+                const bf16x8 bfr = fragS(Ssl, wv * 16 + cl, kk * 4 + q);
+#pragma unroll
+                for (int i = 0; i < 4; i++) {
+                    const bf16x8 af = frag8(BufA, i * 16 + cl, kk * 4 + q);
+                    acc2[i] = __builtin_amdgcn_mfma_f32_16x16x32_bf16(af, bfr, acc2[i], 0, 0, 0);
+                }
+            }
+        }
+        denp[tid] = dacc;
+        __syncthreads();
+
+        stage4h(Cp + 64, BufA, FF, tid);
+        stage4h(Cp + 128, BufA + 4096, FF, tid);
+        pv4(BufB, QF, acc2, wv, cl, q);
+        __syncthreads();
+        stage4h(Cp + 192, BufB, FF, tid);
+        pv4(BufA, QF + 4096, acc2, wv, cl, q);
+        pv4(BufA + 4096, QF + 8192, acc2, wv, cl, q);
+        if (tid < 64)
+            den_l[tid] = rows_part[tid] + denp[4 * tid] + denp[4 * tid + 1] +
+                         denp[4 * tid + 2] + denp[4 * tid + 3];
+        __syncthreads();
+        pv4(BufB, QF + 12288, acc2, wv, cl, q);
+
+        const float dinv = 1.0f / den_l[wv * 16 + cl];
+#pragma unroll
+        for (int i = 0; i < 4; i++)
+#pragma unroll
+            for (int r = 0; r < 4; r++) {
+                const int e = i * 16 + q * 4 + r;
+                Ssl[(wv * 16 + cl) * 68 + e] = f2bf(acc2[i][r] * dinv);
+            }
+        __syncthreads();
+#pragma unroll
+        for (int p = 0; p < 4; p++) {
+            const int idx = p * 256 + tid;
+            const int row = idx >> 4, e4 = idx & 15;
+            ushort4 o = *(const ushort4*)&Ssl[row * 68 + e4 * 4];
+            *(ushort4*)(attnb + ((size_t)(bb * NSEQ + q0 + row)) * DIMM + h * 64 + e4 * 4) = o;
+        }
+    }
+    gbar(bar, 2, NBLK, tid);
+
     {
-        const int drow = tid >> 2, dq = tid & 3;
-        const ushort_t* QQ = QF + dq * 4096;
-#pragma unroll
-        for (int gi = 0; gi < 8; gi++) {
-            const ushort_t* gp = QQ + ((size_t)drow * 8 + (gi ^ (drow & 7))) * 8;
-            const int kbase = dq * 64 + gi * 8;
-#pragma unroll
-            for (int e2 = 0; e2 < 8; e2++)
-                dacc = fmaf(bf2f(gp[e2]), zeps[kbase + e2], dacc);
-        }
-    }
-    __syncthreads();
-
-    floatx4 acc2[4];
-#pragma unroll
-    for (int i = 0; i < 4; i++) acc2[i] = zero;
-    if (hq) {
-#pragma unroll
-        for (int kk = 0; kk < 4; kk++) {
-            const bf16x8 bfr = fragS(Ssl, wv * 16 + cl, kk * 4 + q);
-#pragma unroll
-            for (int i = 0; i < 4; i++) {
-                const bf16x8 af = fragS(BufA, i * 16 + cl, kk * 4 + q);
-                acc2[i] = __builtin_amdgcn_mfma_f32_16x16x32_bf16(af, bfr, acc2[i], 0, 0, 0);
-            }
-        }
-    } else {
-#pragma unroll
-        for (int kk = 0; kk < 2; kk++) {
-            const bf16x8 bfr = fragS(Ssl, wv * 16 + cl, kk * 4 + q);
-#pragma unroll
-            for (int i = 0; i < 4; i++) {
-                const bf16x8 af = frag8(BufA, i * 16 + cl, kk * 4 + q);
-                acc2[i] = __builtin_amdgcn_mfma_f32_16x16x32_bf16(af, bfr, acc2[i], 0, 0, 0);
-            }
-        }
-    }
-    denp[tid] = dacc;
-    __syncthreads();
-
-    stage4h(Cp + 64, BufA, FF, tid);
-    stage4h(Cp + 128, BufA + 4096, FF, tid);
-    pv4(BufB, QF, acc2, wv, cl, q);
-    __syncthreads();
-    stage4h(Cp + 192, BufB, FF, tid);
-    pv4(BufA, QF + 4096, acc2, wv, cl, q);
-    pv4(BufA + 4096, QF + 8192, acc2, wv, cl, q);
-    if (tid < 64)
-        den_l[tid] = rows_part[tid] + denp[4 * tid] + denp[4 * tid + 1] +
-                     denp[4 * tid + 2] + denp[4 * tid + 3];
-    __syncthreads();
-    pv4(BufB, QF + 12288, acc2, wv, cl, q);
-
-    const float dinv = 1.0f / den_l[wv * 16 + cl];
-#pragma unroll
-    for (int i = 0; i < 4; i++)
-#pragma unroll
-        for (int r = 0; r < 4; r++) {
-            const int e = i * 16 + q * 4 + r;
-            Ssl[(wv * 16 + cl) * 68 + e] = f2bf(acc2[i][r] * dinv);
-        }
-    __syncthreads();
-#pragma unroll
-    for (int p = 0; p < 4; p++) {
-        const int idx = p * 256 + tid;
-        const int row = idx >> 4, e4 = idx & 15;
-        ushort4 o = *(const ushort4*)&Ssl[row * 68 + e4 * 4];
-        *(ushort4*)(attnb + ((size_t)(bb * NSEQ + q0 + row)) * DIMM + h * 64 + e4 * 4) = o;
+        ushort_t* A0 = (ushort_t*)SMEM;
+        ushort_t* A1 = (ushort_t*)(SMEM + 8192);
+        ushort_t* B0 = (ushort_t*)(SMEM + 16384);
+        ushort_t* B1 = (ushort_t*)(SMEM + 24576);
+        const int n0 = (bid & 7) * 64, m0 = (bid >> 3) * 64;
+        const ushort_t* AG = attnb + (size_t)m0 * DIMM;
+        const ushort_t* BG = Wto + (size_t)n0 * DIMM;
+
+        floatx4 acc[2][2];
+#pragma unroll
+        for (int i = 0; i < 2; i++)
+#pragma unroll
+            for (int j = 0; j < 2; j++) acc[i][j] = zero;
+        const int wm = (wid >> 1) * 32, wn = (wid & 1) * 32;
+
+        stage4h(AG, A0, DIMM, tid);
+        stage4h(BG, B0, DIMM, tid);
+        __syncthreads();
+        for (int tt = 0; tt < 4; tt++) {
+            const int k0 = tt * 128;
+            stage4h(AG + k0 + 64, A1, DIMM, tid);
+            stage4h(BG + k0 + 64, B1, DIMM, tid);
+            mm22(A0, B0, acc, wm, wn, cl, q);
+            __syncthreads();
+            if (tt < 3) {
+                stage4h(AG + k0 + 128, A0, DIMM, tid);
+                stage4h(BG + k0 + 128, B0, DIMM, tid);
+            }
+            mm22(A1, B1, acc, wm, wn, cl, q);
+            __syncthreads();
+        }
+
+#pragma unroll
+        for (int i = 0; i < 2; i++)
+#pragma unroll
+            for (int j = 0; j < 2; j++) {
+                const int col = n0 + wn + j * 16 + cl;
+                const float bv = bias[col];
+#pragma unroll
+                for (int r = 0; r < 4; r++) {
+                    const int row = m0 + wm + i * 16 + q * 4 + r;
+                    out[(size_t)row * DIMM + col] = acc[i][j][r] + bv;
+                }
+            }
     }
 }
 
@@ -857,11 +871,7 @@
                        x, proj, Wq, Wk, Wv, Wo, xb, projb, Wtq, Wtk, Wtv, Wto, mk_u);
     hipLaunchKernelGGL(gemm_qkv, dim3(384), dim3(256), 0, stream,
                        xb, Wtq, Wtk, Wtv, projb, qb, kb, vTb, mk_u);
-    hipLaunchKernelGGL(featk, dim3(32, 8, 2), dim3(256), 0, stream,
-                       kb, projb, mk_u, vTb, kfb, CTXT, Ksum);
-    hipLaunchKernelGGL(prefix_zs, dim3(1040), dim3(256), 0, stream,
-                       Ksum, Zout, CTXT, ctxp, Sout);
-    hipLaunchKernelGGL(chunk_out_half, dim3(512), dim3(256), 0, stream,
-                       qb, projb, kfb, vTb, Ksum, ctxp, attnb);
-    hipLaunchKernelGGL(gemm_out, dim3(4, 64), dim3(256), 0, stream, attnb, Wto, out, bo);
-}
+    hipLaunchKernelGGL(tail_fused, dim3(512), dim3(256), 0, stream,
+                       kb, projb, mk_u, vTb, kfb, CTXT, Ksum, Zout, ctxp, Sout,
+                       qb, attnb, Wto, out, bo, mk_u + 16);
+}
```

After: 504.1 us. 272% more time.
